# Kernel optimization log

Hardware: AMD Instinct MI355X
Metric: run time of the kernel (lower is better)

Reference implementation:

```python
import jax, jax.numpy as jnp
import numpy as np


def setup_inputs() -> dict:
    key = jax.random.key(0)
    k1, k2, k3, k4, k5, k6 = jax.random.split(key, 6)
    B, N, T, F = 16, 256, 64, 128  # batch, num_hnodes==in_dim==out_dim, time_win, feat
    x = jax.random.normal(k1, (B, N, T, F), dtype=jnp.float32)
    entryid = jax.random.randint(k2, (B, N, T), 0, N, dtype=jnp.int64)
    jobid = jax.random.randint(k3, (B, N, T), 0, 8, dtype=jnp.int64)
    rackid = jax.random.randint(k4, (B, N, T), 0, 16, dtype=jnp.int64)
    full_weight = jax.random.normal(k5, (N, N), dtype=jnp.float32) * 0.05
    bias = jax.random.normal(k6, (N,), dtype=jnp.float32) * 0.01
    gamma = jnp.ones((N,), dtype=jnp.float32)
    beta = jnp.zeros((N,), dtype=jnp.float32)
    return {"x": x, "entryid": entryid, "jobid": jobid, "rackid": rackid,
            "full_weight": full_weight, "bias": bias, "gamma": gamma, "beta": beta}


def reference(x, entryid, jobid, rackid, full_weight, bias, gamma, beta):
    # NOTE: in the original torch module the LayerNorm output is overwritten
    # (y = x.permute(...)) and MaskLinear never adds its bias; we reproduce
    # that exact math, so norm/bias are dead w.r.t. the output.
    B, N, T, F = x.shape  # N == in_dim == out_dim == num_hnodes, T == time_win
    out_features = full_weight.shape[0]

    inp = jnp.transpose(x, (0, 2, 3, 1))  # [B, T, F, N]

    # gather per-(batch,node,time) weight columns: [out, B, N, T]
    weight = full_weight[:, entryid.reshape(-1)].reshape(out_features, B, N, T)

    # job-equality mask: [B, N, N, T] -> permuted to [N, B, N, T]
    same_job = (jobid[:, :, None, :] == jobid[:, None, :, :]) \
               & (jobid[:, :, None, :] != 0) & (jobid[:, None, :, :] != 0)
    mask = jnp.transpose(same_job, (1, 0, 2, 3)).astype(x.dtype)

    masked_weight = weight * mask  # [out(=N), B, N, T] via broadcast over dim0

    # einsum 'bijk,lbki->bijl' with i=T, j=F, k=N, l=out
    y = jnp.einsum('bijk,lbki->bijl', inp, masked_weight)
    y = jax.nn.relu(y)            # dropout is identity at eval
    y = jnp.transpose(y, (0, 3, 1, 2))  # [B, out, T, F]
    return x + y
```

## Files before the change

kernel.cpp:

```cpp
#include <hip/hip_runtime.h>
#include <stdint.h>

typedef float  f32x4 __attribute__((ext_vector_type(4)));
typedef short  s16x8 __attribute__((ext_vector_type(8)));
typedef short  s16x4 __attribute__((ext_vector_type(4)));
typedef unsigned int uint32;

#define B_ 16
#define N_ 256
#define T_ 64
#define F_ 128
#define KT 32
#define NT 8

#define BLKSTR 544
#define X_TILE_STR (16 * BLKSTR)
#define X_OFF 0
#define W_OFF (NT * X_TILE_STR)
#define W_BUF_STR (32 * BLKSTR)
#define E_OFF (W_OFF + 2 * W_BUF_STR)
#define J_OFF (E_OFF + N_ * 4)
#define LDS_SZ (J_OFF + N_)

#define TRREAD(dst, addr) \
  asm volatile("ds_read_b64_tr_b16 %0, %1" : "=v"(dst) : "v"(addr))

#define LGKM_FENCE() asm volatile("s_waitcnt lgkmcnt(0)" ::: "memory")
#define BAR()                                    \
  do {                                           \
    LGKM_FENCE();                                \
    __builtin_amdgcn_s_barrier();                \
    asm volatile("" ::: "memory");               \
  } while (0)

__device__ __forceinline__ unsigned short f2bf(float f) {
  union { float f; unsigned int u; } v; v.f = f;
  unsigned int u = v.u;
  return (unsigned short)((u + 0x7fffu + ((u >> 16) & 1u)) >> 16);
}
__device__ __forceinline__ float bf2f(unsigned short h) {
  union { unsigned int u; float f; } v; v.u = ((unsigned int)h) << 16;
  return v.f;
}

__global__ void wtrans_kernel(const float* __restrict__ fw,
                              unsigned short* __restrict__ fwTb) {
  int c = blockIdx.x;
  int l = threadIdx.x;
  fwTb[c * N_ + l] = f2bf(fw[l * N_ + c]);
}

__global__ __launch_bounds__(512, 2) void fused_kernel(
    const float* __restrict__ x,
    const int* __restrict__ entry,
    const int* __restrict__ job,
    const unsigned short* __restrict__ fwTb,
    float* __restrict__ out) {
  __shared__ __align__(16) char smem[LDS_SZ];
  const uint32 lds_u = (uint32)(uintptr_t)(&smem[0]);

  const int tid = threadIdx.x;
  const int bid = blockIdx.x;
  const int b = bid >> 6;
  const int t = bid & 63;

  int e_val = 0, j_val = 0;
  if (tid < N_) {
    const int idx = (b * N_ + tid) * T_ + t;
    e_val = entry[idx];
    j_val = job[idx];
  }

  const int xk  = tid >> 4;
  const int xf0 = (tid & 15) << 3;
  const float* xsrc = x + ((b * N_ + xk) * T_ + t) * F_ + xf0;
#define XLD(i)                                                            \
  f32x4 q##i##a = *(const f32x4*)(xsrc + (i) * (KT * T_ * F_));           \
  f32x4 q##i##b = *(const f32x4*)(xsrc + (i) * (KT * T_ * F_) + 4);
  XLD(0) XLD(1) XLD(2) XLD(3) XLD(4) XLD(5) XLD(6) XLD(7)
#undef XLD

  if (tid < N_) {
    *(int*)(smem + E_OFF + 4 * tid) = e_val;
    smem[J_OFF + tid] = (char)j_val;
  }
  BAR();

  const int wk  = tid & 31;
  const int wlg = tid >> 5;
  s16x8 gv0, gv1;
  unsigned char gjk;
  {
    const int ev = *(const int*)(smem + E_OFF + 4 * wk);
    gjk = (unsigned char)smem[J_OFF + wk];
    const unsigned short* wrow = fwTb + ev * N_ + wlg * 16;
    gv0 = *(const s16x8*)(wrow);
    gv1 = *(const s16x8*)(wrow + 8);
  }

  const uint64_t jl80 = *(const uint64_t*)(smem + J_OFF + wlg * 16);
  const uint64_t jl81 = *(const uint64_t*)(smem + J_OFF + wlg * 16 + 8);

  const uint32 xdst_in = (uint32)((((xk >> 4) * 8 + (xf0 >> 4)) * BLKSTR) +
                                  ((xk & 15) * 32) + ((xf0 & 15) * 2));
#define XST(i)                                                            \
  {                                                                       \
    s16x8 pk;                                                             \
    _Pragma("unroll") for (int _j = 0; _j < 4; ++_j) {                    \
      pk[_j]     = (short)f2bf(q##i##a[_j]);                              \
      pk[_j + 4] = (short)f2bf(q##i##b[_j]);                              \
    }                                                                     \
    *(s16x8*)(smem + X_OFF + (i) * X_TILE_STR + xdst_in) = pk;            \
  }
  XST(0) XST(1) XST(2) XST(3) XST(4) XST(5) XST(6) XST(7)
#undef XST

  const uint32 wwr_base =
      (uint32)(((wk >> 4) * 16 + wlg) * BLKSTR + (wk & 15) * 32);
  {
    s16x8 m0, m1;
#pragma unroll
    for (int i = 0; i < 8; ++i) {
      const unsigned char a0 = (unsigned char)(jl80 >> (8 * i));
      const unsigned char a1 = (unsigned char)(jl81 >> (8 * i));
      m0[i] = (gjk != 0 && a0 == gjk) ? gv0[i] : (short)0;
      m1[i] = (gjk != 0 && a1 == gjk) ? gv1[i] : (short)0;
    }
    *(s16x8*)(smem + W_OFF + wwr_base) = m0;
    *(s16x8*)(smem + W_OFF + wwr_base + 16) = m1;
  }
  BAR();

  const int lane = tid & 63;
  const int wid  = tid >> 6;
  const int wl   = wid & 3;
  const int wf   = wid >> 2;

  f32x4 acc[4][4];
#pragma unroll
  for (int i = 0; i < 4; ++i)
#pragma unroll
    for (int j = 0; j < 4; ++j) acc[i][j] = (f32x4){0.f, 0.f, 0.f, 0.f};

  for (int kt = 0; kt < NT; ++kt) {
    s16x8 pv0, pv1;
    unsigned char pjk = 0;
    if (kt + 1 < NT) {
      const int k = (kt + 1) * KT + wk;
      const int ev = *(const int*)(smem + E_OFF + 4 * k);
      pjk = (unsigned char)smem[J_OFF + k];
      const unsigned short* wrow = fwTb + ev * N_ + wlg * 16;
      pv0 = *(const s16x8*)(wrow);
      pv1 = *(const s16x8*)(wrow + 8);
    }

    {
      s16x4 ah[4][2], bh[4][2];
      const uint32 wbase =
          lds_u + W_OFF + (uint32)((kt & 1) * W_BUF_STR) + (uint32)(lane * 8);
      const uint32 xbase =
          lds_u + X_OFF + (uint32)(kt * X_TILE_STR) + (uint32)(lane * 8);
#pragma unroll
      for (int li = 0; li < 4; ++li) {
        TRREAD(ah[li][0], wbase + (uint32)((wl * 4 + li) * BLKSTR));
        TRREAD(ah[li][1], wbase + (uint32)((16 + wl * 4 + li) * BLKSTR));
      }
#pragma unroll
      for (int fi = 0; fi < 4; ++fi) {
        TRREAD(bh[fi][0], xbase + (uint32)((wf * 4 + fi) * BLKSTR));
        TRREAD(bh[fi][1], xbase + (uint32)((8 + wf * 4 + fi) * BLKSTR));
      }
      LGKM_FENCE();
      __builtin_amdgcn_sched_barrier(0);
#pragma unroll
      for (int li = 0; li < 4; ++li) {
        s16x8 af = __builtin_shufflevector(ah[li][0], ah[li][1],
                                           0, 1, 2, 3, 4, 5, 6, 7);
#pragma unroll
        for (int fi = 0; fi < 4; ++fi) {
          s16x8 bf = __builtin_shufflevector(bh[fi][0], bh[fi][1],
                                             0, 1, 2, 3, 4, 5, 6, 7);
          acc[li][fi] =
              __builtin_amdgcn_mfma_f32_16x16x32_bf16(af, bf, acc[li][fi], 0, 0, 0);
        }
      }
      __builtin_amdgcn_sched_barrier(0);
    }

    if (kt + 1 < NT) {
      s16x8 m0, m1;
#pragma unroll
      for (int i = 0; i < 8; ++i) {
        const unsigned char a0 = (unsigned char)(jl80 >> (8 * i));
        const unsigned char a1 = (unsigned char)(jl81 >> (8 * i));
        m0[i] = (pjk != 0 && a0 == pjk) ? pv0[i] : (short)0;
        m1[i] = (pjk != 0 && a1 == pjk) ? pv1[i] : (short)0;
      }
      char* wb = smem + W_OFF + ((kt + 1) & 1) * W_BUF_STR + wwr_base;
      *(s16x8*)(wb) = m0;
      *(s16x8*)(wb + 16) = m1;
      BAR();
    }
  }

  const int g4   = (lane >> 4) * 4;
  const int fcol = lane & 15;
#pragma unroll
  for (int li = 0; li < 4; ++li) {
    const int Lb = wl * 4 + li;
    const uint32 rb = lds_u + X_OFF + (uint32)((Lb >> 1) * X_TILE_STR +
                       ((Lb & 1) * 8) * BLKSTR + lane * 8);
    s16x4 xr[4];
#pragma unroll
    for (int fi = 0; fi < 4; ++fi) {
      TRREAD(xr[fi], rb + (uint32)((wf * 4 + fi) * BLKSTR));
    }
    LGKM_FENCE();
    __builtin_amdgcn_sched_barrier(0);
    const int l0 = Lb * 16 + g4;
#pragma unroll
    for (int fi = 0; fi < 4; ++fi) {
      const int f = (wf * 4 + fi) * 16 + fcol;
      float* op = out + ((b * N_ + l0) * T_ + t) * F_ + f;
#pragma unroll
      for (int r = 0; r < 4; ++r) {
        float y = acc[li][fi][r];
        y = y > 0.f ? y : 0.f;
        op[r * (T_ * F_)] = bf2f((unsigned short)xr[fi][r]) + y;
      }
    }
  }
}

extern "C" void kernel_launch(void* const* d_in, const int* in_sizes, int n_in,
                              void* d_out, int out_size, void* d_ws,
                              size_t ws_size, hipStream_t stream) {
  (void)in_sizes; (void)n_in; (void)out_size; (void)ws_size;
  const float* x     = (const float*)d_in[0];
  const int*   entry = (const int*)d_in[1];
  const int*   job   = (const int*)d_in[2];
  const float* fw    = (const float*)d_in[4];
  unsigned short* fwTb = (unsigned short*)d_ws;

  hipLaunchKernelGGL(wtrans_kernel, dim3(N_), dim3(N_), 0, stream, fw, fwTb);
  hipLaunchKernelGGL(fused_kernel, dim3(B_ * T_), dim3(512), 0, stream,
                     x, entry, job, (const unsigned short*)fwTb, (float*)d_out);
}
```

Baseline: 76.88 us.

## Shrink LDS footprint to raise occupancy: single W buffer, register-held ids, unpadded tiles

Drops the LDS staging of entry/job ids and instead has each thread load its needed ids straight from global memory into registers, packed as bytes. The W tile goes from double-buffered to single-buffered, with an extra barrier after the LDS reads so it can be overwritten, and the 544-byte padded block stride becomes 512. Launch bounds go from 2 to 4 blocks per CU. Less LDS per block is meant to allow more resident blocks and better latency hiding. The cost is an extra barrier per K step, possible LDS bank conflicts from removing the padding, more redundant global loads of job ids, and higher register pressure under the tighter launch bound.

```diff
diff --git a/kernel.cpp b/kernel.cpp
--- a/kernel.cpp
+++ b/kernel.cpp
@@ -13,14 +13,11 @@
 #define KT 32
 #define NT 8
 
-#define BLKSTR 544
-#define X_TILE_STR (16 * BLKSTR)
+#define SUBT 512
+#define X_TILE_STR (16 * SUBT)
 #define X_OFF 0
 #define W_OFF (NT * X_TILE_STR)
-#define W_BUF_STR (32 * BLKSTR)
-#define E_OFF (W_OFF + 2 * W_BUF_STR)
-#define J_OFF (E_OFF + N_ * 4)
-#define LDS_SZ (J_OFF + N_)
+#define LDS_SZ (W_OFF + 32 * SUBT)
 
 #define TRREAD(dst, addr) \
   asm volatile("ds_read_b64_tr_b16 %0, %1" : "=v"(dst) : "v"(addr))
@@ -50,7 +47,7 @@
   fwTb[c * N_ + l] = f2bf(fw[l * N_ + c]);
 }
 
-__global__ __launch_bounds__(512, 2) void fused_kernel(
+__global__ __launch_bounds__(512, 4) void fused_kernel(
     const float* __restrict__ x,
     const int* __restrict__ entry,
     const int* __restrict__ job,
@@ -64,12 +61,18 @@
   const int b = bid >> 6;
   const int t = bid & 63;
 
-  int e_val = 0, j_val = 0;
-  if (tid < N_) {
-    const int idx = (b * N_ + tid) * T_ + t;
-    e_val = entry[idx];
-    j_val = job[idx];
-  }
+  const int wk  = tid & 31;
+  const int wlg = tid >> 5;
+
+  int er[8], jr[8], jlr[16];
+#pragma unroll
+  for (int i = 0; i < 8; ++i) {
+    er[i] = entry[(b * N_ + i * KT + wk) * T_ + t];
+    jr[i] = job[(b * N_ + i * KT + wk) * T_ + t];
+  }
+#pragma unroll
+  for (int i = 0; i < 16; ++i)
+    jlr[i] = job[(b * N_ + wlg * 16 + i) * T_ + t];
 
   const int xk  = tid >> 4;
   const int xf0 = (tid & 15) << 3;
@@ -80,28 +83,42 @@
   XLD(0) XLD(1) XLD(2) XLD(3) XLD(4) XLD(5) XLD(6) XLD(7)
 #undef XLD
 
-  if (tid < N_) {
-    *(int*)(smem + E_OFF + 4 * tid) = e_val;
-    smem[J_OFF + tid] = (char)j_val;
-  }
-  BAR();
-
-  const int wk  = tid & 31;
-  const int wlg = tid >> 5;
-  s16x8 gv0, gv1;
-  unsigned char gjk;
+  uint32 ep0 = 0, ep1 = 0, jp0 = 0, jp1 = 0;
+#pragma unroll
+  for (int i = 0; i < 4; ++i) {
+    ep0 |= ((uint32)(er[i] & 255)) << (8 * i);
+    ep1 |= ((uint32)(er[i + 4] & 255)) << (8 * i);
+    jp0 |= ((uint32)(jr[i] & 255)) << (8 * i);
+    jp1 |= ((uint32)(jr[i + 4] & 255)) << (8 * i);
+  }
+  uint64_t jl80 = 0, jl81 = 0;
+#pragma unroll
+  for (int i = 0; i < 8; ++i) {
+    jl80 |= ((uint64_t)(jlr[i] & 255)) << (8 * i);
+    jl81 |= ((uint64_t)(jlr[i + 8] & 255)) << (8 * i);
+  }
+
+  const uint32 wwr_base =
+      (uint32)(((wk >> 4) * 16 + wlg) * SUBT + (wk & 15) * 32);
   {
-    const int ev = *(const int*)(smem + E_OFF + 4 * wk);
-    gjk = (unsigned char)smem[J_OFF + wk];
+    const int ev = (int)(ep0 & 255);
+    const unsigned char gjk = (unsigned char)(jp0 & 255);
     const unsigned short* wrow = fwTb + ev * N_ + wlg * 16;
-    gv0 = *(const s16x8*)(wrow);
-    gv1 = *(const s16x8*)(wrow + 8);
-  }
-
-  const uint64_t jl80 = *(const uint64_t*)(smem + J_OFF + wlg * 16);
-  const uint64_t jl81 = *(const uint64_t*)(smem + J_OFF + wlg * 16 + 8);
-
-  const uint32 xdst_in = (uint32)((((xk >> 4) * 8 + (xf0 >> 4)) * BLKSTR) +
+    s16x8 gv0 = *(const s16x8*)(wrow);
+    s16x8 gv1 = *(const s16x8*)(wrow + 8);
+    s16x8 m0, m1;
+#pragma unroll
+    for (int i = 0; i < 8; ++i) {
+      const unsigned char a0 = (unsigned char)(jl80 >> (8 * i));
+      const unsigned char a1 = (unsigned char)(jl81 >> (8 * i));
+      m0[i] = (gjk != 0 && a0 == gjk) ? gv0[i] : (short)0;
+      m1[i] = (gjk != 0 && a1 == gjk) ? gv1[i] : (short)0;
+    }
+    *(s16x8*)(smem + W_OFF + wwr_base) = m0;
+    *(s16x8*)(smem + W_OFF + wwr_base + 16) = m1;
+  }
+
+  const uint32 xdst_in = (uint32)((((xk >> 4) * 8 + (xf0 >> 4)) * SUBT) +
                                   ((xk & 15) * 32) + ((xf0 & 15) * 2));
 #define XST(i)                                                            \
   {                                                                       \
@@ -114,21 +131,6 @@
   }
   XST(0) XST(1) XST(2) XST(3) XST(4) XST(5) XST(6) XST(7)
 #undef XST
-
-  const uint32 wwr_base =
-      (uint32)(((wk >> 4) * 16 + wlg) * BLKSTR + (wk & 15) * 32);
-  {
-    s16x8 m0, m1;
-#pragma unroll
-    for (int i = 0; i < 8; ++i) {
-      const unsigned char a0 = (unsigned char)(jl80 >> (8 * i));
-      const unsigned char a1 = (unsigned char)(jl81 >> (8 * i));
-      m0[i] = (gjk != 0 && a0 == gjk) ? gv0[i] : (short)0;
-      m1[i] = (gjk != 0 && a1 == gjk) ? gv1[i] : (short)0;
-    }
-    *(s16x8*)(smem + W_OFF + wwr_base) = m0;
-    *(s16x8*)(smem + W_OFF + wwr_base + 16) = m1;
-  }
   BAR();
 
   const int lane = tid & 63;
@@ -146,46 +148,49 @@
     s16x8 pv0, pv1;
     unsigned char pjk = 0;
     if (kt + 1 < NT) {
-      const int k = (kt + 1) * KT + wk;
-      const int ev = *(const int*)(smem + E_OFF + 4 * k);
-      pjk = (unsigned char)smem[J_OFF + k];
+      const uint32 esel = (kt + 1 < 4) ? ep0 : ep1;
+      const uint32 jsel = (kt + 1 < 4) ? jp0 : jp1;
+      const int sh = ((kt + 1) & 3) * 8;
+      const int ev = (int)((esel >> sh) & 255);
+      pjk = (unsigned char)((jsel >> sh) & 255);
       const unsigned short* wrow = fwTb + ev * N_ + wlg * 16;
       pv0 = *(const s16x8*)(wrow);
       pv1 = *(const s16x8*)(wrow + 8);
     }
 
+    s16x4 ah[4][2], bh[4][2];
     {
-      s16x4 ah[4][2], bh[4][2];
-      const uint32 wbase =
-          lds_u + W_OFF + (uint32)((kt & 1) * W_BUF_STR) + (uint32)(lane * 8);
+      const uint32 wbase = lds_u + W_OFF + (uint32)(lane * 8);
       const uint32 xbase =
           lds_u + X_OFF + (uint32)(kt * X_TILE_STR) + (uint32)(lane * 8);
 #pragma unroll
       for (int li = 0; li < 4; ++li) {
-        TRREAD(ah[li][0], wbase + (uint32)((wl * 4 + li) * BLKSTR));
-        TRREAD(ah[li][1], wbase + (uint32)((16 + wl * 4 + li) * BLKSTR));
+        TRREAD(ah[li][0], wbase + (uint32)((wl * 4 + li) * SUBT));
+        TRREAD(ah[li][1], wbase + (uint32)((16 + wl * 4 + li) * SUBT));
       }
 #pragma unroll
       for (int fi = 0; fi < 4; ++fi) {
-        TRREAD(bh[fi][0], xbase + (uint32)((wf * 4 + fi) * BLKSTR));
-        TRREAD(bh[fi][1], xbase + (uint32)((8 + wf * 4 + fi) * BLKSTR));
+        TRREAD(bh[fi][0], xbase + (uint32)((wf * 4 + fi) * SUBT));
+        TRREAD(bh[fi][1], xbase + (uint32)((8 + wf * 4 + fi) * SUBT));
       }
       LGKM_FENCE();
       __builtin_amdgcn_sched_barrier(0);
-#pragma unroll
-      for (int li = 0; li < 4; ++li) {
-        s16x8 af = __builtin_shufflevector(ah[li][0], ah[li][1],
+    }
+    if (kt + 1 < NT) BAR();
+
+#pragma unroll
+    for (int li = 0; li < 4; ++li) {
+      s16x8 af = __builtin_shufflevector(ah[li][0], ah[li][1],
+                                         0, 1, 2, 3, 4, 5, 6, 7);
+#pragma unroll
+      for (int fi = 0; fi < 4; ++fi) {
+        s16x8 bf = __builtin_shufflevector(bh[fi][0], bh[fi][1],
                                            0, 1, 2, 3, 4, 5, 6, 7);
-#pragma unroll
-        for (int fi = 0; fi < 4; ++fi) {
-          s16x8 bf = __builtin_shufflevector(bh[fi][0], bh[fi][1],
-                                             0, 1, 2, 3, 4, 5, 6, 7);
-          acc[li][fi] =
-              __builtin_amdgcn_mfma_f32_16x16x32_bf16(af, bf, acc[li][fi], 0, 0, 0);
-        }
-      }
-      __builtin_amdgcn_sched_barrier(0);
-    }
+        acc[li][fi] =
+            __builtin_amdgcn_mfma_f32_16x16x32_bf16(af, bf, acc[li][fi], 0, 0, 0);
+      }
+    }
+    __builtin_amdgcn_sched_barrier(0);
 
     if (kt + 1 < NT) {
       s16x8 m0, m1;
@@ -196,9 +201,8 @@
         m0[i] = (pjk != 0 && a0 == pjk) ? pv0[i] : (short)0;
         m1[i] = (pjk != 0 && a1 == pjk) ? pv1[i] : (short)0;
       }
-      char* wb = smem + W_OFF + ((kt + 1) & 1) * W_BUF_STR + wwr_base;
-      *(s16x8*)(wb) = m0;
-      *(s16x8*)(wb + 16) = m1;
+      *(s16x8*)(smem + W_OFF + wwr_base) = m0;
+      *(s16x8*)(smem + W_OFF + wwr_base + 16) = m1;
       BAR();
     }
   }
@@ -209,11 +213,11 @@
   for (int li = 0; li < 4; ++li) {
     const int Lb = wl * 4 + li;
     const uint32 rb = lds_u + X_OFF + (uint32)((Lb >> 1) * X_TILE_STR +
-                       ((Lb & 1) * 8) * BLKSTR + lane * 8);
+                       ((Lb & 1) * 8) * SUBT + lane * 8);
     s16x4 xr[4];
 #pragma unroll
     for (int fi = 0; fi < 4; ++fi) {
-      TRREAD(xr[fi], rb + (uint32)((wf * 4 + fi) * BLKSTR));
+      TRREAD(xr[fi], rb + (uint32)((wf * 4 + fi) * SUBT));
     }
     LGKM_FENCE();
     __builtin_amdgcn_sched_barrier(0);
```

Result: slower. 205.2 us (+166.9%).
